# Optimization experiments

Hardware: AMD Instinct MI355X
Metric: run time of the kernel (lower is better)

The kernel has to match this reference:

```python
import jax, jax.numpy as jnp
import numpy as np
import math

H = 12          # num_attention_heads
DH = 64         # attention_head_size
D = H * DH      # hidden_size = 768
LN_EPS = 1e-5
GAUSS_W = 0.3989422804014327
WIDS = [None, 0.1, 1.0, 5.0]


def gauss_weight(L, wid):
    # faithful to generate_gauss_weight: row-normalized Gaussian bump per query pos
    center = (jnp.arange(L, dtype=jnp.float32) / L)[:, None]       # (L,1)
    pos = jnp.linspace(0.0, 1.0, L, dtype=jnp.float32)[None, :]    # (1,L)
    width = max(wid, 0.01) / 9.0                                   # static python scalar
    g = (GAUSS_W / width) * jnp.exp(-(pos - center) ** 2 / (2.0 * width * width))
    return g / jnp.max(g, axis=-1, keepdims=True)                  # (L,L)


def layer_norm(x, g, b):
    mu = jnp.mean(x, axis=-1, keepdims=True)
    var = jnp.mean((x - mu) ** 2, axis=-1, keepdims=True)
    return (x - mu) * jax.lax.rsqrt(var + LN_EPS) * g + b


def bert_attention(x, mask, qkv_w, qkv_b, out_w, out_b, ln_g, ln_b, wid):
    # x: (N,L,D); mask: (N,L,L); qkv_w: (3,D,D); qkv_b: (3,D)
    N, L, _ = x.shape

    def heads(t):  # (N,L,D) -> (N,H,L,DH)
        return t.reshape(N, L, H, DH).transpose(0, 2, 1, 3)

    q = heads(x @ qkv_w[0] + qkv_b[0])
    k = heads(x @ qkv_w[1] + qkv_b[1])
    v = heads(x @ qkv_w[2] + qkv_b[2])

    scores = jnp.einsum('nhqd,nhkd->nhqk', q, k) / math.sqrt(DH)   # (N,H,L,L)
    if wid is not None:
        scores = scores * gauss_weight(L, wid)[None, None]          # multiplicative GMM mask
    scores = scores + (1.0 - mask[:, None, :, :]) * -10000.0
    probs = jax.nn.softmax(scores, axis=-1)                         # dropout = identity (eval)
    ctx = jnp.einsum('nhqk,nhkd->nhqd', probs, v)                   # (N,H,L,DH)
    ctx = ctx.transpose(0, 2, 1, 3).reshape(N, L, D)

    proj = ctx @ out_w + out_b
    return layer_norm(proj + x, ln_g, ln_b)


def setup_inputs() -> dict:
    key = jax.random.key(0)
    ks = jax.random.split(key, 4)
    N, L = 4, 1024
    s = 0.02
    return {
        'input_tensor': jax.random.normal(ks[0], (N, L, D), dtype=jnp.float32),
        'attention_mask': jnp.ones((N, L, L), dtype=jnp.float32),
        'qkv_w': jax.random.normal(ks[1], (4, 3, D, D), dtype=jnp.float32) * s,
        'qkv_b': jnp.zeros((4, 3, D), dtype=jnp.float32),
        'out_w': jax.random.normal(ks[2], (4, D, D), dtype=jnp.float32) * s,
        'out_b': jnp.zeros((4, D), dtype=jnp.float32),
        'ln_g': jnp.ones((4, D), dtype=jnp.float32),
        'ln_b': jnp.zeros((4, D), dtype=jnp.float32),
    }


def reference(input_tensor, attention_mask, qkv_w, qkv_b, out_w, out_b, ln_g, ln_b):
    # pure_block=False path: 4 parallel GMM-masked attention branches, averaged
    outs = [
        bert_attention(input_tensor, attention_mask,
                       qkv_w[i], qkv_b[i], out_w[i], out_b[i], ln_g[i], ln_b[i], WIDS[i])
        for i in range(4)
    ]
    return jnp.mean(jnp.stack(outs, axis=-1), axis=-1)
```

## Files before the change

kernel.cpp:

```cpp
#include <hip/hip_runtime.h>
#include <hip/hip_bf16.h>

#define NB 4
#define LQ 1024
#define NH 12
#define DHD 64
#define DM 768
#define MTOT (NB*LQ)
#define L2E 1.4426950408889634f
#define SMB 11.541560327111708f
#define CFAR 3.3546262790251185e-4f

typedef __attribute__((ext_vector_type(4))) float f32x4;
typedef __attribute__((ext_vector_type(8))) short bf16x8;
typedef __attribute__((ext_vector_type(4))) short short4v;
typedef unsigned short u16;

#if __has_builtin(__builtin_amdgcn_exp2f)
#define EXP2(x) __builtin_amdgcn_exp2f(x)
#else
#define EXP2(x) __expf((x) * 0.6931471805599453f)
#endif

#define VMCNT(n) asm volatile("s_waitcnt vmcnt(" #n ")" ::: "memory")
#define RAW_BAR() __builtin_amdgcn_s_barrier()

__device__ __forceinline__ u16 f2bf(float f){
  union { float f; unsigned int i; } v; v.f = f;
  unsigned int r = v.i + 0x7FFFu + ((v.i >> 16) & 1u);
  return (u16)(r >> 16);
}
__device__ __forceinline__ float bf2f(u16 u){
  union { unsigned int i; float f; } v; v.i = ((unsigned int)u) << 16;
  return v.f;
}
__device__ __forceinline__ unsigned cvt_pk_bf16(float lo, float hi){
  unsigned r;
  asm("v_cvt_pk_bf16_f32 %0, %1, %2" : "=v"(r) : "v"(lo), "v"(hi));
  return r;
}

typedef const __attribute__((address_space(1))) void* gas_t;
typedef __attribute__((address_space(3))) void* las_t;
__device__ __forceinline__ void gload16(const void* g, void* l){
  __builtin_amdgcn_global_load_lds((gas_t)g, (las_t)l, 16, 0, 0);
}

__global__ void k_cvt_x(const float* __restrict__ x, u16* __restrict__ xb){
  int i = (blockIdx.x * 256 + threadIdx.x) * 4;
  float4 v = *reinterpret_cast<const float4*>(x + i);
  short4v o;
  o[0] = (short)f2bf(v.x); o[1] = (short)f2bf(v.y);
  o[2] = (short)f2bf(v.z); o[3] = (short)f2bf(v.w);
  *reinterpret_cast<short4v*>(xb + i) = o;
}

__global__ void k_wt(const float* __restrict__ qkv_w, const float* __restrict__ out_w,
                     u16* __restrict__ wt){
  int mat = blockIdx.z;
  const float* W = (mat < 12) ? (qkv_w + (size_t)mat*DM*DM)
                              : (out_w + (size_t)(mat-12)*DM*DM);
  __shared__ float tile[32][33];
  int j0 = blockIdx.x*32, k0 = blockIdx.y*32;
  int tx = threadIdx.x, ty = threadIdx.y;
  #pragma unroll
  for (int i=0;i<4;i++)
    tile[ty + i*8][tx] = W[(size_t)(k0 + ty + i*8)*DM + j0 + tx];
  __syncthreads();
  u16* dst = wt + (size_t)mat*DM*DM;
  int tid = ty*32 + tx;
  int jj = tid >> 3, kq = tid & 7;
  short4v pk;
  #pragma unroll
  for (int t=0;t<4;t++) pk[t] = (short)f2bf(tile[kq*4 + t][jj]);
  *reinterpret_cast<short4v*>(&dst[(size_t)(j0 + jj)*DM + k0 + kq*4]) = pk;
}

__global__ void k_maskchk(const float* __restrict__ mask, unsigned* __restrict__ flags){
  int qt = blockIdx.x, kt = blockIdx.y, n = blockIdx.z;
  const float* M = mask + ((size_t)(n*LQ) + qt*64)*LQ + kt*64;
  int tid = threadIdx.x;
  int r = tid >> 2, c4 = (tid & 3) * 16;
  int ok = 1;
  #pragma unroll
  for (int j=0;j<4;j++){
    float4 v = *reinterpret_cast<const float4*>(M + (size_t)r*LQ + c4 + j*4);
    ok &= (v.x==1.f) & (v.y==1.f) & (v.z==1.f) & (v.w==1.f);
  }
  __shared__ int sok[4];
  unsigned long long bal = __ballot(ok);
  if ((tid & 63) == 0) sok[tid>>6] = (bal == 0xFFFFFFFFFFFFFFFFull) ? 1 : 0;
  __syncthreads();
  if (tid == 0) flags[((size_t)n*16 + qt)*16 + kt] = sok[0] & sok[1] & sok[2] & sok[3];
}

__global__ __launch_bounds__(256) void k_vsum(const u16* __restrict__ qkvws, float* __restrict__ ps){
  const int nh = blockIdx.x;
  const int b  = blockIdx.y;
  const size_t blk = (size_t)NB*NH*LQ*DHD;
  const u16* Vt = qkvws + (size_t)(b*3+2)*blk + (size_t)nh*DHD*LQ;
  const int tid = threadIdx.x;
  const int dh = tid >> 2, c = tid & 3;
  float* psb = ps + ((size_t)(b*48 + nh)*17)*64;
  float acc = 0.f;
  for (int kt = 0; kt < 16; ++kt){
    if (c == 0) psb[kt*64 + dh] = acc;
    bf16x8 v0 = *reinterpret_cast<const bf16x8*>(&Vt[(size_t)dh*LQ + kt*64 + c*16]);
    bf16x8 v1 = *reinterpret_cast<const bf16x8*>(&Vt[(size_t)dh*LQ + kt*64 + c*16 + 8]);
    float s = 0.f;
    #pragma unroll
    for (int j=0;j<8;j++) s += bf2f((u16)v0[j]) + bf2f((u16)v1[j]);
    s += __shfl_xor(s, 1);
    s += __shfl_xor(s, 2);
    acc += s;
  }
  if (c == 0) psb[16*64 + dh] = acc;
}

__device__ __forceinline__ void gemm_tile32(const u16* __restrict__ Ag,
                                            const u16* __restrict__ Bg,
                                            u16* smem, f32x4 acc[4][4])
{
  const int tid = threadIdx.x, lane = tid & 63, w = tid >> 6;
  const int wr = (w >> 1) * 64, wc = (w & 1) * 64;
  const int rl = lane & 15, q4 = lane >> 4;
  const int srow = tid >> 2;
  const int su = (tid & 3) ^ ((srow >> 1) & 3);

  #define QSTG(buf, k0_) { \
    _Pragma("unroll") \
    for (int r = 0; r < 2; ++r){ \
      gload16(Ag + (size_t)(r*64 + srow)*DM + (k0_) + su*8, smem + (buf)*8192 + r*2048 + tid*8); \
      gload16(Bg + (size_t)(r*64 + srow)*DM + (k0_) + su*8, smem + (buf)*8192 + 4096 + r*2048 + tid*8); \
    } }

  QSTG(0, 0);
  QSTG(1, 32);
  int cur = 0, nxt2 = 2;
  for (int it = 0; it < 24; ++it){
    if (it + 2 < 24){
      QSTG(nxt2, (it+2)*32);
      VMCNT(8);
    } else if (it + 1 < 24){
      VMCNT(4);
    } else {
      VMCNT(0);
    }
    RAW_BAR();
    __builtin_amdgcn_sched_barrier(0);
    const u16* al = smem + cur*8192;
    const u16* bl = al + 4096;
    bf16x8 af[4], bfr[4];
    #pragma unroll
    for (int f = 0; f < 4; ++f){
      int ra = wr + f*16 + rl, rb = wc + f*16 + rl;
      int ua = q4 ^ ((ra >> 1) & 3), ub = q4 ^ ((rb >> 1) & 3);
      af[f]  = *reinterpret_cast<const bf16x8*>(&al[ra*32 + ua*8]);
      bfr[f] = *reinterpret_cast<const bf16x8*>(&bl[rb*32 + ub*8]);
    }
    #pragma unroll
    for (int mf=0; mf<4; ++mf)
      #pragma unroll
      for (int nf=0; nf<4; ++nf)
        acc[mf][nf] = __builtin_amdgcn_mfma_f32_16x16x32_bf16(af[mf], bfr[nf], acc[mf][nf], 0,0,0);
    RAW_BAR();
    cur = cur + 1 == 3 ? 0 : cur + 1;
    nxt2 = nxt2 + 1 == 3 ? 0 : nxt2 + 1;
  }
  #undef QSTG
}

__global__ __launch_bounds__(256) void k_qkv(const u16* __restrict__ xb, const u16* __restrict__ wt,
                     const float* __restrict__ qkv_b, u16* __restrict__ qkvws)
{
  __shared__ __align__(16) u16 smem[24576];
  const int bid = blockIdx.x;
  const int orig = (bid & 7) * 288 + (bid >> 3);
  const int j0 = (orig % 6) * 128;
  const int m0 = ((orig / 6) % 32) * 128;
  const int mat = orig / 192;
  const int t = mat % 3;
  f32x4 acc[4][4] = {};
  gemm_tile32(xb + (size_t)m0*DM, wt + (size_t)mat*DM*DM + (size_t)j0*DM, smem, acc);

  const int tid = threadIdx.x, lane = tid & 63, w = tid >> 6;
  const int wr = (w >> 1) * 64, wc = (w & 1) * 64;
  const int rl = lane & 15, rg = (lane >> 4) * 4;
  const float sc = (t == 0) ? 0.125f : 1.0f;
  const size_t matbase = (size_t)mat * ((size_t)NB*NH*LQ*DHD);
  if (t < 2){
    #pragma unroll
    for (int nf=0; nf<4; ++nf){
      int jc = wc + nf*16 + rl;
      float bias = qkv_b[mat*DM + j0 + jc];
      #pragma unroll
      for (int mf=0; mf<4; ++mf){
        int row = wr + mf*16 + rg;
        #pragma unroll
        for (int i=0;i<4;i++)
          smem[(row+i)*136 + jc] = f2bf((acc[mf][nf][i] + bias) * sc);
      }
    }
    __syncthreads();
    const int n = m0 >> 10, l0 = m0 & 1023;
    const int hbase = j0 >> 6;
    #pragma unroll
    for (int jj=0; jj<8; ++jj){
      int idx = tid + 256*jj;
      int l = idx >> 4, ch = idx & 15;
      bf16x8 v = *reinterpret_cast<const bf16x8*>(&smem[l*136 + ch*8]);
      int hh = hbase + (ch >> 3);
      int dh0 = (ch & 7) * 8;
      *reinterpret_cast<bf16x8*>(
        &qkvws[matbase + ((size_t)(n*NH + hh)*LQ + l0 + l)*DHD + dh0]) = v;
    }
  } else {
    #pragma unroll
    for (int nf=0; nf<4; ++nf){
      int j = j0 + wc + nf*16 + rl;
      float bias = qkv_b[mat*DM + j];
      int h = j >> 6, dh = j & 63;
      #pragma unroll
      for (int mf=0; mf<4; ++mf){
        int mB = m0 + wr + mf*16 + rg;
        int n = mB >> 10, l = mB & 1023;
        short4v pk;
        #pragma unroll
        for (int i=0;i<4;i++) pk[i] = (short)f2bf(acc[mf][nf][i] + bias);
        *reinterpret_cast<short4v*>(&qkvws[matbase + ((size_t)(n*NH + h)*DHD + dh)*LQ + l]) = pk;
      }
    }
  }
}

__global__ __launch_bounds__(512) void k_attn(const u16* __restrict__ qkvws, const float* __restrict__ mask,
                      const unsigned* __restrict__ flags, const float* __restrict__ ps,
                      u16* __restrict__ ctx, float c2_1, float c2_2, float c2_3)
{
  __shared__ __align__(16) u16 kv_lds[2][2][64*64];
  __shared__ __align__(16) u16 p_lds[128*64];
  const int bid = blockIdx.x;
  const int orig = (bid & 7) * 144 + (bid >> 3);
  const int qp = orig & 7;
  const int r  = orig >> 3;
  const int jb = r % 3;
  const int nh = r / 3;
  const int n = nh / NH, h = nh % NH;
  const int tid = threadIdx.x, lane = tid & 63, w = tid >> 6;
  const int wl = w & 3, half = w >> 2;
  const int qt = qp*2 + half;
  const int rl = lane & 15, q4 = lane >> 4, kc8 = q4*8, rg = q4*4;
  const int q0 = qt*64 + wl*16;

  const size_t blk = (size_t)NB*NH*LQ*DHD;
  const float* Mb = mask + (size_t)n*LQ*LQ;

  float dmin2[4], cq[4];
  #pragma unroll
  for (int i=0;i<4;i++){
    int q = q0 + rg + i;
    float c = (float)q * (1.0f/1024.0f);
    float ksf = floorf(c * 1023.0f + 0.5f);
    float dm = ksf * (1.0f/1023.0f) - c;
    cq[i] = c; dmin2[i] = dm*dm;
  }

  int ra_a = 1, ra_b = 1;
  {
    int qa = qp*2, qb = qp*2+1;
    for (int t = 0; t < 16; ++t){
      ra_a &= (flags[((size_t)n*16 + qa)*16 + t] != 0u) ? 1 : 0;
      ra_b &= (flags[((size_t)n*16 + qb)*16 + t] != 0u) ? 1 : 0;
    }
  }
  const int myrowall = half ? ra_b : ra_a;

  const int r8 = tid >> 3;
  const int uu = (tid & 7) ^ (r8 & 7);

  auto pass = [&](const int b, const float c2){
    const bool useG = (b != 0);
    const u16* Qb = qkvws + (size_t)(b*3+0)*blk + (size_t)nh*LQ*DHD;
    const u16* Kb = qkvws + (size_t)(b*3+1)*blk + (size_t)nh*LQ*DHD;
    const u16* Vt = qkvws + (size_t)(b*3+2)*blk + (size_t)nh*DHD*LQ;

    bf16x8 qf0 = *reinterpret_cast<const bf16x8*>(&Qb[(size_t)(q0+rl)*DHD + kc8]);
    bf16x8 qf1 = *reinterpret_cast<const bf16x8*>(&Qb[(size_t)(q0+rl)*DHD + 32 + kc8]);

    float srun[4] = {0.f,0.f,0.f,0.f};
    f32x4 o[4] = {};

    int lo_a = 0, hi_a = 16, lo_b2 = 0, hi_b2 = 16;
    {
      int qa = qp*2, qb = qp*2+1;
      if (ra_a){
        if (b == 1){ lo_a = qa>0?qa-1:0; hi_a = qa<15?qa+2:16; }
        else if (b == 2){ lo_a = qa>5?qa-5:0; hi_a = qa<10?qa+6:16; }
      }
      if (ra_b){
        if (b == 1){ lo_b2 = qb>0?qb-1:0; hi_b2 = qb<15?qb+2:16; }
        else if (b == 2){ lo_b2 = qb>5?qb-5:0; hi_b2 = qb<10?qb+6:16; }
      }
    }
    const int mylo = half ? lo_b2 : lo_a;
    const int myhi = half ? hi_b2 : hi_a;
    const int blo = lo_a < lo_b2 ? lo_a : lo_b2;
    const int bhi = hi_a > hi_b2 ? hi_a : hi_b2;
    const int mynt = myhi - mylo;

    if (myrowall && mynt < 16){
      const float* psb = ps + ((size_t)(b*48 + nh)*17)*64;
      #pragma unroll
      for (int nf=0; nf<4; ++nf){
        int dh = nf*16 + rl;
        float sfar = psb[16*64 + dh] - psb[myhi*64 + dh] + psb[mylo*64 + dh];
        float fv = CFAR * sfar;
        #pragma unroll
        for (int i=0;i<4;i++) o[nf][i] = fv;
      }
      float sinit = CFAR * (float)(64*(16 - mynt));
      #pragma unroll
      for (int i=0;i<4;i++) srun[i] = sinit;
    }

    #define STAGE8(buf, kt_) { \
      gload16(Kb + (size_t)((kt_)*64 + r8)*DHD + uu*8, (u16*)kv_lds[buf][0] + tid*8); \
      gload16(Vt + (size_t)r8*LQ + (kt_)*64 + uu*8, (u16*)kv_lds[buf][1] + tid*8); }

    STAGE8(0, blo);

    const int nloop = bhi - blo;
    for (int it = 0; it < nloop; ++it){
      const int kt = blo + it;
      const int cur = it & 1;
      if (it + 1 < nloop){
        STAGE8(cur^1, kt+1);
        VMCNT(2);
      } else {
        VMCNT(0);
      }
      RAW_BAR();
      __builtin_amdgcn_sched_barrier(0);

      if (kt >= mylo && kt < myhi){
        const bool allones = myrowall || (flags[((size_t)n*16 + qt)*16 + kt] != 0u);
        const u16* kbuf = (const u16*)kv_lds[cur][0];
        const u16* vbuf = (const u16*)kv_lds[cur][1];

        f32x4 sf[4] = {};
        __builtin_amdgcn_s_setprio(1);
        #pragma unroll
        for (int nf=0; nf<4; ++nf){
          int row = nf*16 + rl, sw = (row & 7) << 3;
          bf16x8 kf0 = *reinterpret_cast<const bf16x8*>(&kbuf[row*64 + (kc8 ^ sw)]);
          bf16x8 kf1 = *reinterpret_cast<const bf16x8*>(&kbuf[row*64 + ((32 + kc8) ^ sw)]);
          sf[nf] = __builtin_amdgcn_mfma_f32_16x16x32_bf16(qf0, kf0, sf[nf], 0,0,0);
          sf[nf] = __builtin_amdgcn_mfma_f32_16x16x32_bf16(qf1, kf1, sf[nf], 0,0,0);
        }
        __builtin_amdgcn_s_setprio(0);

        float pv[4][4];
        #pragma unroll
        for (int nf=0; nf<4; ++nf){
          int key = kt*64 + nf*16 + rl;
          float pos = (float)key * (1.0f/1023.0f);
          #pragma unroll
          for (int i=0;i<4;i++){
            float s = sf[nf][i];
            if (useG){
              float d = pos - cq[i];
              float tg = fmaf(-d, d, dmin2[i]);
              s *= EXP2(tg * c2);
            }
            if (!allones){
              int q = q0 + rg + i;
              s = fmaf(1.0f - Mb[(size_t)q*LQ + key], -10000.0f, s);
            }
            float p = EXP2(fmaf(s, L2E, -SMB));
            srun[i] += p;
            pv[nf][i] = p;
          }
        }

        #pragma unroll
        for (int np=0; np<2; ++np)
          #pragma unroll
          for (int i=0;i<4;i++){
            unsigned u = cvt_pk_bf16(pv[np*2][i], pv[np*2+1][i]);
            int row = w*16 + rg + i, sw = (row & 7) << 3;
            p_lds[row*64 + ((np*32 + rl) ^ sw)]      = (u16)(u & 0xffffu);
            p_lds[row*64 + ((np*32 + 16 + rl) ^ sw)] = (u16)(u >> 16);
          }
        asm volatile("s_waitcnt lgkmcnt(0)" ::: "memory");
        __builtin_amdgcn_sched_barrier(0);

        {
          int prow = w*16 + rl, psw = (prow & 7) << 3;
          bf16x8 pa0 = *reinterpret_cast<const bf16x8*>(&p_lds[prow*64 + (kc8 ^ psw)]);
          bf16x8 pa1 = *reinterpret_cast<const bf16x8*>(&p_lds[prow*64 + ((32 + kc8) ^ psw)]);
          __builtin_amdgcn_s_setprio(1);
          #pragma unroll
          for (int nf=0; nf<4; ++nf){
            int row = nf*16 + rl, sw = (row & 7) << 3;
            bf16x8 vv0 = *reinterpret_cast<const bf16x8*>(&vbuf[row*64 + (kc8 ^ sw)]);
            bf16x8 vv1 = *reinterpret_cast<const bf16x8*>(&vbuf[row*64 + ((32 + kc8) ^ sw)]);
            o[nf] = __builtin_amdgcn_mfma_f32_16x16x32_bf16(pa0, vv0, o[nf], 0,0,0);
            o[nf] = __builtin_amdgcn_mfma_f32_16x16x32_bf16(pa1, vv1, o[nf], 0,0,0);
          }
          __builtin_amdgcn_s_setprio(0);
        }
      }
      RAW_BAR();
    }
    #undef STAGE8

    #pragma unroll
    for (int off=1; off<16; off<<=1){
      #pragma unroll
      for (int i=0;i<4;i++) srun[i] += __shfl_xor(srun[i], off);
    }
    #pragma unroll
    for (int i=0;i<4;i++){
      float inv = 1.0f / (srun[i] + 1e-35f);
      int q = q0 + rg + i;
      size_t mrow = ((size_t)(n*LQ + q)) * DM;
      #pragma unroll
      for (int nf=0; nf<4; ++nf){
        int d = h*DHD + nf*16 + rl;
        ctx[(size_t)b*((size_t)MTOT*DM) + mrow + d] = f2bf(o[nf][i] * inv);
      }
    }
  };

  if (jb == 0){ pass(0, 0.f); pass(1, c2_1); }
  else if (jb == 1){ pass(2, c2_2); }
  else { pass(3, c2_3); }
}

__global__ __launch_bounds__(256) void k_proj(const u16* __restrict__ ctx, const u16* __restrict__ wt,
                      const float* __restrict__ out_b, u16* __restrict__ proj)
{
  __shared__ __align__(16) u16 smem[24576];
  const int bid = blockIdx.x;
  const int orig = (bid & 7) * 96 + (bid >> 3);
  const int j0 = (orig % 6) * 128;
  const int m0 = ((orig / 6) % 32) * 128;
  const int b = orig / 192;
  f32x4 acc[4][4] = {};
  gemm_tile32(ctx + (size_t)b*MTOT*DM + (size_t)m0*DM,
              wt + (size_t)(12+b)*DM*DM + (size_t)j0*DM, smem, acc);
  const int tid = threadIdx.x, lane = tid & 63, w = tid >> 6;
  const int wr = (w >> 1) * 64, wc = (w & 1) * 64;
  const int rl = lane & 15, rg = (lane >> 4) * 4;
  #pragma unroll
  for (int nf=0; nf<4; ++nf){
    int jc = wc + nf*16 + rl;
    float bias = out_b[b*DM + j0 + jc];
    #pragma unroll
    for (int mf=0; mf<4; ++mf){
      int row = wr + mf*16 + rg;
      #pragma unroll
      for (int i=0;i<4;i++)
        smem[(row+i)*136 + jc] = f2bf(acc[mf][nf][i] + bias);
    }
  }
  __syncthreads();
  #pragma unroll
  for (int jj=0; jj<8; ++jj){
    int idx = tid + 256*jj;
    int l = idx >> 4, ch = idx & 15;
    bf16x8 v = *reinterpret_cast<const bf16x8*>(&smem[l*136 + ch*8]);
    *reinterpret_cast<bf16x8*>(&proj[((size_t)b*MTOT + m0 + l)*DM + j0 + ch*8]) = v;
  }
}

__global__ __launch_bounds__(256) void k_ln(const float* __restrict__ x, const u16* __restrict__ proj,
                    const float* __restrict__ ln_g, const float* __restrict__ ln_b,
                    float* __restrict__ out)
{
  const int m = blockIdx.x;
  const int tid = threadIdx.x, lane = tid & 63, w = tid >> 6;
  __shared__ float rb[4][2][4];
  float xr[3], acc[3] = {0.f,0.f,0.f};
  #pragma unroll
  for (int c=0;c<3;c++) xr[c] = x[(size_t)m*DM + tid + c*256];
  float vv[4][3], s1[4], s2[4];
  #pragma unroll
  for (int b=0;b<4;b++){
    s1[b] = 0.f; s2[b] = 0.f;
    #pragma unroll
    for (int c=0;c<3;c++){
      float v = bf2f(proj[((size_t)b*MTOT + m)*DM + tid + c*256]) + xr[c];
      vv[b][c] = v; s1[b] += v; s2[b] += v*v;
    }
  }
  #pragma unroll
  for (int b=0;b<4;b++){
    #pragma unroll
    for (int off=32; off>=1; off>>=1){
      s1[b] += __shfl_xor(s1[b], off);
      s2[b] += __shfl_xor(s2[b], off);
    }
    if (lane == 0){ rb[b][0][w] = s1[b]; rb[b][1][w] = s2[b]; }
  }
  __syncthreads();
  #pragma unroll
  for (int b=0;b<4;b++){
    float S1 = rb[b][0][0]+rb[b][0][1]+rb[b][0][2]+rb[b][0][3];
    float S2 = rb[b][1][0]+rb[b][1][1]+rb[b][1][2]+rb[b][1][3];
    float mu = S1 * (1.0f/768.0f);
    float var = S2 * (1.0f/768.0f) - mu*mu;
    float rs = rsqrtf(var + 1e-5f);
    #pragma unroll
    for (int c=0;c<3;c++){
      int j = tid + c*256;
      acc[c] += 0.25f * ((vv[b][c]-mu)*rs*ln_g[b*DM+j] + ln_b[b*DM+j]);
    }
  }
  #pragma unroll
  for (int c=0;c<3;c++) out[(size_t)m*DM + tid + c*256] = acc[c];
}

extern "C" void kernel_launch(void* const* d_in, const int* in_sizes, int n_in,
                              void* d_out, int out_size, void* d_ws, size_t ws_size,
                              hipStream_t stream)
{
  const float* x     = (const float*)d_in[0];
  const float* mask  = (const float*)d_in[1];
  const float* qkv_w = (const float*)d_in[2];
  const float* qkv_b = (const float*)d_in[3];
  const float* out_w = (const float*)d_in[4];
  const float* out_b = (const float*)d_in[5];
  const float* ln_g  = (const float*)d_in[6];
  const float* ln_b  = (const float*)d_in[7];
  float* out = (float*)d_out;
  char* ws = (char*)d_ws;

  u16* xb        = (u16*)(ws);
  unsigned* flags= (unsigned*)(ws);
  float* ps      = (float*)(ws + 8192);
  u16* wt        = (u16*)(ws + 6291456);
  u16* qkv       = (u16*)(ws + 25165824);
  u16* ctx       = (u16*)(ws + 100663296);
  u16* proj      = (u16*)(ws + 25165824);

  float c2[3];
  const float wid[3] = {0.1f, 1.0f, 5.0f};
  for (int i=0;i<3;i++){
    float wdt = wid[i]/9.0f;
    c2[i] = (1.0f/(2.0f*wdt*wdt)) * L2E;
  }

  k_cvt_x<<<dim3(3072), dim3(256), 0, stream>>>(x, xb);
  k_wt<<<dim3(24,24,16), dim3(32,8), 0, stream>>>(qkv_w, out_w, wt);
  k_qkv<<<dim3(2304), dim3(256), 0, stream>>>(xb, wt, qkv_b, qkv);
  k_vsum<<<dim3(48,4), dim3(256), 0, stream>>>(qkv, ps);
  k_maskchk<<<dim3(16,16,4), dim3(256), 0, stream>>>(mask, flags);
  k_attn<<<dim3(1152), dim3(512), 0, stream>>>(qkv, mask, flags, ps, ctx, c2[0], c2[1], c2[2]);
  k_proj<<<dim3(768), dim3(256), 0, stream>>>(ctx, wt, out_b, proj);
  k_ln<<<dim3(4096), dim3(256), 0, stream>>>(x, proj, ln_g, ln_b, out);
}
```

Before: 231.8 us.

## Compute transposed scores so P stays in registers, dropping LDS round-trip

```diff
diff --git a/kernel.cpp b/kernel.cpp
--- a/kernel.cpp
+++ b/kernel.cpp
@@ -238,7 +238,6 @@
                       u16* __restrict__ ctx, float c2_1, float c2_2, float c2_3)
 {
   __shared__ __align__(16) u16 kv_lds[2][2][64*64];
-  __shared__ __align__(16) u16 p_lds[128*64];
   const int bid = blockIdx.x;
   const int orig = (bid & 7) * 144 + (bid >> 3);
   const int qp = orig & 7;
@@ -251,18 +250,17 @@
   const int qt = qp*2 + half;
   const int rl = lane & 15, q4 = lane >> 4, kc8 = q4*8, rg = q4*4;
   const int q0 = qt*64 + wl*16;
+  const int myq = q0 + rl;
 
   const size_t blk = (size_t)NB*NH*LQ*DHD;
   const float* Mb = mask + (size_t)n*LQ*LQ;
 
-  float dmin2[4], cq[4];
-  #pragma unroll
-  for (int i=0;i<4;i++){
-    int q = q0 + rg + i;
-    float c = (float)q * (1.0f/1024.0f);
+  float cq, dmin2;
+  {
+    float c = (float)myq * (1.0f/1024.0f);
     float ksf = floorf(c * 1023.0f + 0.5f);
     float dm = ksf * (1.0f/1023.0f) - c;
-    cq[i] = c; dmin2[i] = dm*dm;
+    cq = c; dmin2 = dm*dm;
   }
 
   int ra_a = 1, ra_b = 1;
@@ -284,11 +282,11 @@
     const u16* Kb = qkvws + (size_t)(b*3+1)*blk + (size_t)nh*LQ*DHD;
     const u16* Vt = qkvws + (size_t)(b*3+2)*blk + (size_t)nh*DHD*LQ;
 
-    bf16x8 qf0 = *reinterpret_cast<const bf16x8*>(&Qb[(size_t)(q0+rl)*DHD + kc8]);
-    bf16x8 qf1 = *reinterpret_cast<const bf16x8*>(&Qb[(size_t)(q0+rl)*DHD + 32 + kc8]);
-
-    float srun[4] = {0.f,0.f,0.f,0.f};
-    f32x4 o[4] = {};
+    bf16x8 qf0 = *reinterpret_cast<const bf16x8*>(&Qb[(size_t)myq*DHD + kc8]);
+    bf16x8 qf1 = *reinterpret_cast<const bf16x8*>(&Qb[(size_t)myq*DHD + 32 + kc8]);
+
+    float srun = 0.f;
+    f32x4 o2[4] = {};
 
     int lo_a = 0, hi_a = 16, lo_b2 = 0, hi_b2 = 16;
     {
@@ -311,16 +309,17 @@
     if (myrowall && mynt < 16){
       const float* psb = ps + ((size_t)(b*48 + nh)*17)*64;
       #pragma unroll
-      for (int nf=0; nf<4; ++nf){
-        int dh = nf*16 + rl;
-        float sfar = psb[16*64 + dh] - psb[myhi*64 + dh] + psb[mylo*64 + dh];
-        float fv = CFAR * sfar;
-        #pragma unroll
-        for (int i=0;i<4;i++) o[nf][i] = fv;
-      }
-      float sinit = CFAR * (float)(64*(16 - mynt));
-      #pragma unroll
-      for (int i=0;i<4;i++) srun[i] = sinit;
+      for (int nfp=0; nfp<4; ++nfp){
+        int dh0 = nfp*16 + rg;
+        float4 tA = *reinterpret_cast<const float4*>(&psb[16*64 + dh0]);
+        float4 tH = *reinterpret_cast<const float4*>(&psb[myhi*64 + dh0]);
+        float4 tL = *reinterpret_cast<const float4*>(&psb[mylo*64 + dh0]);
+        o2[nfp][0] = CFAR * (tA.x - tH.x + tL.x);
+        o2[nfp][1] = CFAR * (tA.y - tH.y + tL.y);
+        o2[nfp][2] = CFAR * (tA.z - tH.z + tL.z);
+        o2[nfp][3] = CFAR * (tA.w - tH.w + tL.w);
+      }
+      srun = CFAR * (float)(64*(16 - mynt));
     }
 
     #define STAGE8(buf, kt_) { \
@@ -354,81 +353,78 @@
           int row = nf*16 + rl, sw = (row & 7) << 3;
           bf16x8 kf0 = *reinterpret_cast<const bf16x8*>(&kbuf[row*64 + (kc8 ^ sw)]);
           bf16x8 kf1 = *reinterpret_cast<const bf16x8*>(&kbuf[row*64 + ((32 + kc8) ^ sw)]);
-          sf[nf] = __builtin_amdgcn_mfma_f32_16x16x32_bf16(qf0, kf0, sf[nf], 0,0,0);
-          sf[nf] = __builtin_amdgcn_mfma_f32_16x16x32_bf16(qf1, kf1, sf[nf], 0,0,0);
+          sf[nf] = __builtin_amdgcn_mfma_f32_16x16x32_bf16(kf0, qf0, sf[nf], 0,0,0);
+          sf[nf] = __builtin_amdgcn_mfma_f32_16x16x32_bf16(kf1, qf1, sf[nf], 0,0,0);
         }
         __builtin_amdgcn_s_setprio(0);
 
         float pv[4][4];
         #pragma unroll
         for (int nf=0; nf<4; ++nf){
-          int key = kt*64 + nf*16 + rl;
-          float pos = (float)key * (1.0f/1023.0f);
           #pragma unroll
           for (int i=0;i<4;i++){
+            int key = kt*64 + nf*16 + rg + i;
             float s = sf[nf][i];
             if (useG){
-              float d = pos - cq[i];
-              float tg = fmaf(-d, d, dmin2[i]);
+              float pos = (float)key * (1.0f/1023.0f);
+              float d = pos - cq;
+              float tg = fmaf(-d, d, dmin2);
               s *= EXP2(tg * c2);
             }
             if (!allones){
-              int q = q0 + rg + i;
-              s = fmaf(1.0f - Mb[(size_t)q*LQ + key], -10000.0f, s);
+              s = fmaf(1.0f - Mb[(size_t)myq*LQ + key], -10000.0f, s);
             }
             float p = EXP2(fmaf(s, L2E, -SMB));
-            srun[i] += p;
+            srun += p;
             pv[nf][i] = p;
           }
         }
 
+        union { unsigned u[4]; bf16x8 v; } pk0, pk1;
+        pk0.u[0] = cvt_pk_bf16(pv[0][0], pv[0][1]);
+        pk0.u[1] = cvt_pk_bf16(pv[0][2], pv[0][3]);
+        pk0.u[2] = cvt_pk_bf16(pv[1][0], pv[1][1]);
+        pk0.u[3] = cvt_pk_bf16(pv[1][2], pv[1][3]);
+        pk1.u[0] = cvt_pk_bf16(pv[2][0], pv[2][1]);
+        pk1.u[1] = cvt_pk_bf16(pv[2][2], pv[2][3]);
+        pk1.u[2] = cvt_pk_bf16(pv[3][0], pv[3][1]);
+        pk1.u[3] = cvt_pk_bf16(pv[3][2], pv[3][3]);
+
+        __builtin_amdgcn_s_setprio(1);
         #pragma unroll
-        for (int np=0; np<2; ++np)
+        for (int nfp=0; nfp<4; ++nfp){
+          int row = nfp*16 + rl;
+          int sw = row & 7;
           #pragma unroll
-          for (int i=0;i<4;i++){
-            unsigned u = cvt_pk_bf16(pv[np*2][i], pv[np*2+1][i]);
-            int row = w*16 + rg + i, sw = (row & 7) << 3;
-            p_lds[row*64 + ((np*32 + rl) ^ sw)]      = (u16)(u & 0xffffu);
-            p_lds[row*64 + ((np*32 + 16 + rl) ^ sw)] = (u16)(u >> 16);
+          for (int hh=0; hh<2; ++hh){
+            int c0 = hh*32 + rg;
+            int c1 = c0 + 16;
+            union { short4v s4[2]; bf16x8 v; } va;
+            va.s4[0] = *reinterpret_cast<const short4v*>(
+                &vbuf[row*64 + (((c0 >> 3) ^ sw) << 3) + (c0 & 7)]);
+            va.s4[1] = *reinterpret_cast<const short4v*>(
+                &vbuf[row*64 + (((c1 >> 3) ^ sw) << 3) + (c1 & 7)]);
+            o2[nfp] = __builtin_amdgcn_mfma_f32_16x16x32_bf16(
+                va.v, hh ? pk1.v : pk0.v, o2[nfp], 0,0,0);
           }
-        asm volatile("s_waitcnt lgkmcnt(0)" ::: "memory");
-        __builtin_amdgcn_sched_barrier(0);
-
-        {
-          int prow = w*16 + rl, psw = (prow & 7) << 3;
-          bf16x8 pa0 = *reinterpret_cast<const bf16x8*>(&p_lds[prow*64 + (kc8 ^ psw)]);
-          bf16x8 pa1 = *reinterpret_cast<const bf16x8*>(&p_lds[prow*64 + ((32 + kc8) ^ psw)]);
-          __builtin_amdgcn_s_setprio(1);
-          #pragma unroll
-          for (int nf=0; nf<4; ++nf){
-            int row = nf*16 + rl, sw = (row & 7) << 3;
-            bf16x8 vv0 = *reinterpret_cast<const bf16x8*>(&vbuf[row*64 + (kc8 ^ sw)]);
-            bf16x8 vv1 = *reinterpret_cast<const bf16x8*>(&vbuf[row*64 + ((32 + kc8) ^ sw)]);
-            o[nf] = __builtin_amdgcn_mfma_f32_16x16x32_bf16(pa0, vv0, o[nf], 0,0,0);
-            o[nf] = __builtin_amdgcn_mfma_f32_16x16x32_bf16(pa1, vv1, o[nf], 0,0,0);
-          }
-          __builtin_amdgcn_s_setprio(0);
         }
+        __builtin_amdgcn_s_setprio(0);
       }
       RAW_BAR();
     }
     #undef STAGE8
 
-    #pragma unroll
-    for (int off=1; off<16; off<<=1){
+    srun += __shfl_xor(srun, 16);
+    srun += __shfl_xor(srun, 32);
+    float inv = 1.0f / (srun + 1e-35f);
+    size_t mrow = ((size_t)(n*LQ + myq)) * DM;
+    #pragma unroll
+    for (int nfp=0; nfp<4; ++nfp){
+      short4v pk;
       #pragma unroll
-      for (int i=0;i<4;i++) srun[i] += __shfl_xor(srun[i], off);
-    }
-    #pragma unroll
-    for (int i=0;i<4;i++){
-      float inv = 1.0f / (srun[i] + 1e-35f);
-      int q = q0 + rg + i;
-      size_t mrow = ((size_t)(n*LQ + q)) * DM;
-      #pragma unroll
-      for (int nf=0; nf<4; ++nf){
-        int d = h*DHD + nf*16 + rl;
-        ctx[(size_t)b*((size_t)MTOT*DM) + mrow + d] = f2bf(o[nf][i] * inv);
-      }
+      for (int i=0;i<4;i++) pk[i] = (short)f2bf(o2[nfp][i] * inv);
+      *reinterpret_cast<short4v*>(
+        &ctx[(size_t)b*((size_t)MTOT*DM) + mrow + h*DHD + nfp*16 + rg]) = pk;
     }
   };
 
```

Result: slower. 239.4 us (+3.2%).
